# Kernel optimization log

Measured on AMD Instinct MI355X. Metric: run time of the kernel, lower is better.

The kernel has to match this reference:

```python
import jax, jax.numpy as jnp
import numpy as np

B, N_OBJS, HW = 2, 30, 64
W_H = HW * HW                      # 4096 visual tokens
N = W_H + 4 * N_OBJS + 64          # 4280 total tokens (satisfies the N - 4*n_objs - 64 == 64*64 check)
QUERY_DIM, HEADS, DIM_HEAD = 320, 8, 40
INNER = HEADS * DIM_HEAD


def setup_inputs() -> dict:
    key = jax.random.key(0)
    ks = jax.random.split(key, 7)
    x = jax.random.normal(ks[0], (B, N, QUERY_DIM), dtype=jnp.float32)
    # binary per-object instance masks on the 64x64 visual grid
    att_masks = (jax.random.uniform(ks[1], (B, N_OBJS, HW, HW)) < 0.15).astype(jnp.float32)
    s = 0.02
    Wq = jax.random.normal(ks[2], (QUERY_DIM, INNER), dtype=jnp.float32) * s
    Wk = jax.random.normal(ks[3], (QUERY_DIM, INNER), dtype=jnp.float32) * s
    Wv = jax.random.normal(ks[4], (QUERY_DIM, INNER), dtype=jnp.float32) * s
    Wo = jax.random.normal(ks[5], (INNER, QUERY_DIM), dtype=jnp.float32) * s
    bo = jax.random.normal(ks[6], (QUERY_DIM,), dtype=jnp.float32) * s
    return {"x": x, "att_masks": att_masks, "Wq": Wq, "Wk": Wk, "Wv": Wv, "Wo": Wo, "bo": bo}


def _build_mask(att_masks):
    # att_masks: [B, n_objs, 64, 64] -> additive/boolean grounding mask [B, 1, N, N]
    b, n_objs = att_masks.shape[0], att_masks.shape[1]
    m = att_masks.reshape(b, n_objs, W_H)                     # [B, O, 4096]
    # sum over objects of per-object outer products (bmm then sum over objs)
    ind = jnp.einsum('boi,boj->bij', m, m)                    # [B, 4096, 4096]
    # visual_token_masks ends up exactly 1 where ind>=1 else 0 (the two masked assigns)
    visual = (ind >= 1.0).astype(att_masks.dtype)
    mask = jnp.ones((b, 1, N, N), dtype=att_masks.dtype)
    mask = mask.at[:, :, :W_H, :W_H].set(visual[:, None])
    mr = m[:, None]                                           # [B, 1, O, 4096]
    rep_rows = jnp.tile(mr, (1, 1, 4, 1))                     # [B, 1, 4O, 4096]
    mask = mask.at[:, :, W_H:N - 64, :W_H].set(rep_rows)
    mask = mask.at[:, :, W_H + n_objs:W_H + 3 * n_objs, :W_H].set(1.0)
    rep_cols = jnp.tile(jnp.swapaxes(mr, 2, 3), (1, 1, 1, 4))  # [B, 1, 4096, 4O]
    mask = mask.at[:, :, :W_H, W_H:N - 64].set(rep_cols)
    mask = mask.at[:, :, :W_H, W_H + n_objs:W_H + 3 * n_objs].set(1.0)
    mask = mask + jnp.eye(N, dtype=att_masks.dtype)[None, None] * 1e-9
    return mask


def reference(x, att_masks, Wq, Wk, Wv, Wo, bo):
    b, n, _ = x.shape
    scale = DIM_HEAD ** -0.5
    q = (x @ Wq).reshape(b, n, HEADS, DIM_HEAD).transpose(0, 2, 1, 3)  # [B,H,N,C]
    k = (x @ Wk).reshape(b, n, HEADS, DIM_HEAD).transpose(0, 2, 1, 3)
    v = (x @ Wv).reshape(b, n, HEADS, DIM_HEAD).transpose(0, 2, 1, 3)
    mask = _build_mask(att_masks)                                      # [B,1,N,N]
    sim = jnp.einsum('bhic,bhjc->bhij', q, k) * scale                  # [B,H,N,N]
    sim = jnp.where(mask <= 0.0, -jnp.inf, sim)
    attn = jax.nn.softmax(sim, axis=-1)
    out = jnp.einsum('bhij,bhjc->bhic', attn, v)                       # [B,H,N,C]
    out = out.transpose(0, 2, 1, 3).reshape(b, n, INNER)
    return out @ Wo + bo
```

## Files before the change

kernel.cpp:

```cpp
#include <hip/hip_runtime.h>
#include <hip/hip_bf16.h>

#define BB 2
#define N_TOK 4280
#define NPAD 4352
#define MPAD 8576
#define WH 4096
#define NOBJ 30
#define QDIM 320
#define HEADS 8
#define DHEAD 40
#define M_ROWS (BB * N_TOK)
#define NT64 (NPAD / 64)
#define NQT (NPAD / 128)
#define KSPLIT 4
#define NTH (NT64 / KSPLIT)

typedef __attribute__((ext_vector_type(8))) short short8;
typedef __attribute__((ext_vector_type(4))) short short4v;
typedef __attribute__((ext_vector_type(4))) float f32x4;
typedef __attribute__((ext_vector_type(4))) unsigned uintx4;
typedef __attribute__((ext_vector_type(2))) unsigned long long u64x2;

#define GLD16(lds, g) __builtin_amdgcn_global_load_lds( \
    (const __attribute__((address_space(1))) unsigned*)(g), \
    (__attribute__((address_space(3))) unsigned*)(lds), 16, 0, 0)
#define GLD4(lds, g) __builtin_amdgcn_global_load_lds( \
    (const __attribute__((address_space(1))) unsigned*)(g), \
    (__attribute__((address_space(3))) unsigned*)(lds), 4, 0, 0)

__device__ __forceinline__ ushort f2bf(float x) {
    union { __hip_bfloat16 h; ushort u; } cv;
    cv.h = __float2bfloat16(x);
    return cv.u;
}
__device__ __forceinline__ float bf2f(ushort u) {
    union { unsigned u; float f; } cv;
    cv.u = ((unsigned)u) << 16;
    return cv.f;
}

__global__ void k_zero(u64x2* __restrict__ p, int n16) {
    int stride = gridDim.x * blockDim.x;
    u64x2 z = {0ull, 0ull};
    for (int i = blockIdx.x * blockDim.x + threadIdx.x; i < n16; i += stride)
        p[i] = z;
}

__global__ void k_bits(const float* __restrict__ att, unsigned* __restrict__ bits) {
    int gid = blockIdx.x * blockDim.x + threadIdx.x;
    if (gid >= BB * NPAD) return;
    int b = gid / NPAD, i = gid - b * NPAD;
    unsigned v = 0;
    if (i < WH) {
        const float* base = att + (size_t)b * NOBJ * WH + i;
        #pragma unroll
        for (int o = 0; o < NOBJ; ++o)
            if (base[(size_t)o * WH] > 0.5f) v |= (1u << o);
    }
    bits[gid] = v;
}

__global__ void k_xcvt(const float* __restrict__ x, ushort* __restrict__ xb) {
    int i = blockIdx.x * blockDim.x + threadIdx.x;
    if (i >= M_ROWS * QDIM / 8) return;
    float4 v0 = ((const float4*)x)[i * 2];
    float4 v1 = ((const float4*)x)[i * 2 + 1];
    short8 o;
    o[0] = (short)f2bf(v0.x); o[1] = (short)f2bf(v0.y);
    o[2] = (short)f2bf(v0.z); o[3] = (short)f2bf(v0.w);
    o[4] = (short)f2bf(v1.x); o[5] = (short)f2bf(v1.y);
    o[6] = (short)f2bf(v1.z); o[7] = (short)f2bf(v1.w);
    ((short8*)xb)[i] = o;
}

__global__ __launch_bounds__(256) void k_wcvt(const float* __restrict__ Wq,
                                              const float* __restrict__ Wk,
                                              const float* __restrict__ Wv,
                                              const float* __restrict__ Wo,
                                              ushort* __restrict__ WtAll) {
    __shared__ float T[32][33];
    const int k0 = blockIdx.x * 32;
    const int np0 = blockIdx.y * 32;
    const float SC = 0.15811388300841897f * 1.4426950408889634f;
    const float* src; int n0; float sc = 1.f;
    if (np0 < 320)      { src = Wq; n0 = np0;       sc = SC; }
    else if (np0 < 640) { src = Wk; n0 = np0 - 320; }
    else if (np0 < 960) { src = Wv; n0 = np0 - 640; }
    else                { src = Wo; n0 = np0 - 960; }
    const int tid = threadIdx.x;
    #pragma unroll
    for (int it = 0; it < 4; ++it) {
        int idx = tid + it * 256;
        int r = idx >> 5, c = idx & 31;
        T[r][c] = src[(size_t)(k0 + r) * QDIM + n0 + c];
    }
    __syncthreads();
    #pragma unroll
    for (int it = 0; it < 4; ++it) {
        int idx = tid + it * 256;
        int rr = idx >> 5, cc = idx & 31;
        WtAll[(size_t)(np0 + rr) * QDIM + k0 + cc] = f2bf(T[cc][rr] * sc);
    }
}

template<int IS_OUT>
__global__ __launch_bounds__(256) void k_mm(const ushort* __restrict__ A,
                                            const ushort* __restrict__ Wt,
                                            const float* __restrict__ bias,
                                            ushort* __restrict__ Qb,
                                            ushort* __restrict__ Kb,
                                            ushort* __restrict__ Vt,
                                            float* __restrict__ Cout) {
    __shared__ __align__(16) char Ab[2][8192];
    __shared__ __align__(16) char Bb[2][8192];
    const int tid = threadIdx.x, lane = tid & 63, wv = tid >> 6;
    const int g = lane >> 4, c16 = lane & 15, l7 = lane & 7;
    const int rsub = lane >> 3, slotx = lane & 7;
    const int m0 = blockIdx.x * 64;
    const int nt = blockIdx.y;

    f32x4 acc[4] = {{0,0,0,0},{0,0,0,0},{0,0,0,0},{0,0,0,0}};

    auto STAGE = [&](int ks, int bufi) {
        const int k0 = ks * 64;
        #pragma unroll
        for (int u = 0; u < 2; ++u) {
            int r0 = wv * 16 + u * 8;
            int row = r0 + rsub;
            int slot = slotx ^ (row & 7);
            GLD16(Ab[bufi] + r0 * 128, A + (size_t)(m0 + row) * QDIM + k0 + slot * 8);
            GLD16(Bb[bufi] + r0 * 128, Wt + (size_t)(nt * 64 + row) * QDIM + k0 + slot * 8);
        }
    };

    const int sl0 = (g ^ l7) * 16, sl1 = ((4 + g) ^ l7) * 16;

    STAGE(0, 0);
    __syncthreads();
    int cur = 0;
    for (int ks = 0; ks < 5; ++ks) {
        if (ks < 4) STAGE(ks + 1, cur ^ 1);
        const char* bbase = Bb[cur] + (wv * 16 + c16) * 128;
        short8 bf0 = *(const short8*)(bbase + sl0);
        short8 bf1 = *(const short8*)(bbase + sl1);
        #pragma unroll
        for (int mi = 0; mi < 4; ++mi) {
            const char* abase = Ab[cur] + (mi * 16 + c16) * 128;
            acc[mi] = __builtin_amdgcn_mfma_f32_16x16x32_bf16(*(const short8*)(abase + sl0), bf0, acc[mi], 0, 0, 0);
            acc[mi] = __builtin_amdgcn_mfma_f32_16x16x32_bf16(*(const short8*)(abase + sl1), bf1, acc[mi], 0, 0, 0);
        }
        __syncthreads();
        cur ^= 1;
    }

    const int ng = nt * 64 + wv * 16 + c16;
    if (IS_OUT) {
        float bv = bias[ng];
        #pragma unroll
        for (int mi = 0; mi < 4; ++mi)
            #pragma unroll
            for (int r = 0; r < 4; ++r) {
                int m = m0 + mi * 16 + g * 4 + r;
                if (m < M_ROWS) Cout[(size_t)m * QDIM + ng] = acc[mi][r] + bv;
            }
    } else {
        int p = ng / QDIM, nn = ng - p * QDIM;
        int h = nn / DHEAD, d = nn - h * DHEAD;
        if (p == 2) {
            #pragma unroll
            for (int mi = 0; mi < 4; ++mi) {
                int m = m0 + mi * 16 + g * 4;
                if (m >= M_ROWS) continue;
                int b = m / N_TOK, tok = m - b * N_TOK;
                short4v w4;
                w4[0] = (short)f2bf(acc[mi][0]);
                w4[1] = (short)f2bf(acc[mi][1]);
                w4[2] = (short)f2bf(acc[mi][2]);
                w4[3] = (short)f2bf(acc[mi][3]);
                *(short4v*)(Vt + ((size_t)(b * HEADS + h) * 48 + d) * NPAD + tok) = w4;
            }
        } else {
            ushort* base = (p == 0) ? Qb : Kb;
            #pragma unroll
            for (int mi = 0; mi < 4; ++mi)
                #pragma unroll
                for (int r = 0; r < 4; ++r) {
                    int m = m0 + mi * 16 + g * 4 + r;
                    if (m >= M_ROWS) continue;
                    int b = m / N_TOK, tok = m - b * N_TOK;
                    base[((size_t)(b * HEADS + h) * NPAD + tok) * 64 + d] = f2bf(acc[mi][r]);
                }
        }
    }
}

__global__ __launch_bounds__(256) void k_norm(const ushort* __restrict__ Qb,
                                              const ushort* __restrict__ Kb,
                                              float* __restrict__ Bsh) {
    __shared__ float rq[256], rk[256];
    const int bh = blockIdx.x, tid = threadIdx.x;
    float mq = 0.f, mk = 0.f;
    for (int tok = tid; tok < N_TOK; tok += 256) {
        const ushort* qp = Qb + ((size_t)bh * NPAD + tok) * 64;
        const ushort* kp = Kb + ((size_t)bh * NPAD + tok) * 64;
        float sq = 0.f, sk = 0.f;
        #pragma unroll
        for (int d8 = 0; d8 < 40; d8 += 8) {
            short8 a = *(const short8*)(qp + d8);
            short8 c = *(const short8*)(kp + d8);
            #pragma unroll
            for (int j = 0; j < 8; ++j) {
                float fa = bf2f((ushort)a[j]), fc = bf2f((ushort)c[j]);
                sq += fa * fa; sk += fc * fc;
            }
        }
        mq = fmaxf(mq, sq); mk = fmaxf(mk, sk);
    }
    rq[tid] = mq; rk[tid] = mk;
    __syncthreads();
    for (int s = 128; s > 0; s >>= 1) {
        if (tid < s) {
            rq[tid] = fmaxf(rq[tid], rq[tid + s]);
            rk[tid] = fmaxf(rk[tid], rk[tid + s]);
        }
        __syncthreads();
    }
    if (tid == 0) Bsh[bh] = sqrtf(rq[0]) * sqrtf(rk[0]);
}

__global__ void k_patch(ushort* __restrict__ Qb, ushort* __restrict__ Kb,
                        ushort* __restrict__ Vt, const float* __restrict__ Bsh) {
    int gid = blockIdx.x * blockDim.x + threadIdx.x;
    if (gid >= 16 * NPAD) return;
    int bh = gid / NPAD, tok = gid - bh * NPAD;
    float B = Bsh[bh];
    Qb[(size_t)gid * 64 + 40] = f2bf(-B);
    if (tok < N_TOK) Kb[(size_t)gid * 64 + 40] = (ushort)0x3F80;
    Vt[((size_t)bh * 48 + 40) * NPAD + tok] = (tok < N_TOK) ? (ushort)0x3F80 : (ushort)0;
}

__device__ __forceinline__ bool mask_ok(int i, int j, unsigned bi, unsigned bj) {
    if (j >= N_TOK) return false;
    if (i == j) return true;
    if (i < WH) {
        if (j < WH) return (bi & bj) != 0u;
        if (j >= WH + 4 * NOBJ) return true;
        int cI = j - WH;
        if ((unsigned)(cI - NOBJ) < (unsigned)(2 * NOBJ)) return true;
        int om = (cI < NOBJ) ? cI : cI - 3 * NOBJ;
        return ((bi >> om) & 1u) != 0u;
    }
    if (j >= WH) return true;
    if (i >= WH + 4 * NOBJ) return true;
    int rI = i - WH;
    if ((unsigned)(rI - NOBJ) < (unsigned)(2 * NOBJ)) return true;
    int om = (rI < NOBJ) ? rI : rI - 3 * NOBJ;
    return ((bj >> om) & 1u) != 0u;
}

__global__ __launch_bounds__(256, 4) void k_attn(const ushort* __restrict__ Qb,
                                                 const ushort* __restrict__ Kb,
                                                 const ushort* __restrict__ Vt,
                                                 const unsigned* __restrict__ bits,
                                                 float* __restrict__ Opart,
                                                 float* __restrict__ Lpart) {
    __shared__ __align__(16) char KtB[64 * 128];
    __shared__ __align__(16) char VtB[48 * 128];
    __shared__ __align__(16) char PsB[4 * 4096];
    __shared__ __align__(16) unsigned bJB[64];

    const int tid = threadIdx.x;
    const int lane = tid & 63, wv = tid >> 6;
    const int g = lane >> 4, c16 = lane & 15;
    const int l7x = c16 & 7;
    const int rsub = lane >> 3, slotx = lane & 7;

    const int bid = blockIdx.x;
    const int logical = (bid & 7) * 272 + (bid >> 3);
    const int grp = logical / NQT;
    const int qt = logical - grp * NQT;
    const int bh = grp >> 2, ks = grp & 3;
    const int b = bh >> 3;
    const int qb_blk = qt * 128;
    const int q0w = qb_blk + wv * 32;
    const int iqA = q0w + c16, iqB = iqA + 16;
    const bool vis_i = (qt < 32);
    const int t0 = ks * NTH;

    short8 qA0, qA1, qB0, qB1;
    {
        const ushort* qp = Qb + ((size_t)bh * NPAD + iqA) * 64 + g * 8;
        qA0 = *(const short8*)(qp);
        qA1 = *(const short8*)(qp + 32);
        qB0 = *(const short8*)(qp + 16 * 64);
        qB1 = *(const short8*)(qp + 16 * 64 + 32);
    }
    const unsigned bI_A = bits[(size_t)b * NPAD + iqA];
    const unsigned bI_B = bits[(size_t)b * NPAD + iqB];

    const ushort* kp = Kb + ((size_t)bh * NPAD + t0 * 64 + wv * 16 + rsub) * 64 + (slotx ^ rsub) * 8;
    const ushort* vbase = Vt + (size_t)bh * 48 * NPAD;
    int voff0 = 0, voff1 = 0;
    if (wv < 3) {
        int d0 = wv * 16 + rsub, d1 = d0 + 8;
        voff0 = d0 * NPAD + (slotx ^ rsub) * 8;
        voff1 = d1 * NPAD + (slotx ^ rsub) * 8;
    }
    const unsigned* bp = bits + (size_t)b * NPAD + t0 * 64 + lane;

    auto STAGE_K = [&](const ushort* kpt) {
        GLD16(KtB + (wv * 16) * 128, kpt);
        GLD16(KtB + (wv * 16 + 8) * 128, kpt + 512);
    };
    auto STAGE_V = [&](int j0) {
        if (wv < 3) {
            GLD16(VtB + (wv * 16) * 128, vbase + j0 + voff0);
            GLD16(VtB + (wv * 16 + 8) * 128, vbase + j0 + voff1);
        }
    };
    auto STAGE_B = [&](const unsigned* bpt) {
        if (wv == 3) GLD4(bJB, bpt);
    };

    const int sl0 = (g ^ l7x) * 16;
    const int sl1 = ((4 + g) ^ l7x) * 16;
    const int pswA = wv * 4096 + c16 * 128;
    const int pswB = pswA + 2048;
    const int swz = l7x << 4;

    f32x4 oA0 = {0,0,0,0}, oA1 = oA0, oA2 = oA0;
    f32x4 oB0 = oA0, oB1 = oA0, oB2 = oA0;

    STAGE_K(kp); STAGE_V(t0 * 64); STAGE_B(bp);
    __syncthreads();

    for (int t = 0; t < NTH; ++t) {
        const int tg = t0 + t;
        const int j0 = tg * 64;

        auto do_tile = [&](auto okA_fn, auto okB_fn) {
            #pragma unroll
            for (int kt = 0; kt < 4; ++kt) {
                const char* arow = KtB + (kt * 16 + c16) * 128;
                short8 a0 = *(const short8*)(arow + sl0);
                short8 a1 = *(const short8*)(arow + sl1);
                f32x4 sA = {0,0,0,0}, sB = {0,0,0,0};
                __builtin_amdgcn_s_setprio(1);
                sA = __builtin_amdgcn_mfma_f32_16x16x32_bf16(a0, qA0, sA, 0, 0, 0);
                sA = __builtin_amdgcn_mfma_f32_16x16x32_bf16(a1, qA1, sA, 0, 0, 0);
                sB = __builtin_amdgcn_mfma_f32_16x16x32_bf16(a0, qB0, sB, 0, 0, 0);
                sB = __builtin_amdgcn_mfma_f32_16x16x32_bf16(a1, qB1, sB, 0, 0, 0);
                __builtin_amdgcn_s_setprio(0);
                uintx4 bk = *(const uintx4*)&bJB[kt * 16 + g * 4];
                float pA[4], pB[4];
                #pragma unroll
                for (int r = 0; r < 4; ++r) {
                    int j = j0 + kt * 16 + g * 4 + r;
                    float eA = __builtin_amdgcn_exp2f(sA[r]);
                    float eB = __builtin_amdgcn_exp2f(sB[r]);
                    pA[r] = okA_fn(j, bk[r]) ? eA : 0.f;
                    pB[r] = okB_fn(j, bk[r]) ? eB : 0.f;
                }
                unsigned wA0, wA1, wB0, wB1;
                asm("v_cvt_pk_bf16_f32 %0, %1, %2" : "=v"(wA0) : "v"(pA[0]), "v"(pA[1]));
                asm("v_cvt_pk_bf16_f32 %0, %1, %2" : "=v"(wA1) : "v"(pA[2]), "v"(pA[3]));
                asm("v_cvt_pk_bf16_f32 %0, %1, %2" : "=v"(wB0) : "v"(pB[0]), "v"(pB[1]));
                asm("v_cvt_pk_bf16_f32 %0, %1, %2" : "=v"(wB1) : "v"(pB[2]), "v"(pB[3]));
                uint2 vA; vA.x = wA0; vA.y = wA1;
                uint2 vB; vB.x = wB0; vB.y = wB1;
                int po = (kt * 32 + g * 8) ^ swz;
                *(uint2*)(PsB + pswA + po) = vA;
                *(uint2*)(PsB + pswB + po) = vB;
            }
        };

        const bool vis_j = (j0 + 64 <= WH);
        if (vis_i && vis_j && ((tg >> 1) != qt)) {
            do_tile([&](int j, unsigned bj) { return (bI_A & bj) != 0u; },
                    [&](int j, unsigned bj) { return (bI_B & bj) != 0u; });
        } else if (vis_i && vis_j) {
            do_tile([&](int j, unsigned bj) { return ((bI_A & bj) != 0u) || (iqA == j); },
                    [&](int j, unsigned bj) { return ((bI_B & bj) != 0u) || (iqB == j); });
        } else {
            do_tile([&](int j, unsigned bj) { return mask_ok(iqA, j, bI_A, bj); },
                    [&](int j, unsigned bj) { return mask_ok(iqB, j, bI_B, bj); });
        }

        __syncthreads();
        kp += 64 * 64; bp += 64;
        if (t + 1 < NTH) { STAGE_K(kp); STAGE_B(bp); }

        short8 paA0 = *(const short8*)(PsB + pswA + sl0);
        short8 paA1 = *(const short8*)(PsB + pswA + sl1);
        short8 paB0 = *(const short8*)(PsB + pswB + sl0);
        short8 paB1 = *(const short8*)(PsB + pswB + sl1);
        {
            const char* v0r = VtB + (0 * 16 + c16) * 128;
            const char* v1r = VtB + (1 * 16 + c16) * 128;
            const char* v2r = VtB + (2 * 16 + c16) * 128;
            short8 v00 = *(const short8*)(v0r + sl0), v01 = *(const short8*)(v0r + sl1);
            short8 v10 = *(const short8*)(v1r + sl0), v11 = *(const short8*)(v1r + sl1);
            short8 v20 = *(const short8*)(v2r + sl0), v21 = *(const short8*)(v2r + sl1);
            __builtin_amdgcn_s_setprio(1);
            oA0 = __builtin_amdgcn_mfma_f32_16x16x32_bf16(paA0, v00, oA0, 0, 0, 0);
            oA0 = __builtin_amdgcn_mfma_f32_16x16x32_bf16(paA1, v01, oA0, 0, 0, 0);
            oB0 = __builtin_amdgcn_mfma_f32_16x16x32_bf16(paB0, v00, oB0, 0, 0, 0);
            oB0 = __builtin_amdgcn_mfma_f32_16x16x32_bf16(paB1, v01, oB0, 0, 0, 0);
            oA1 = __builtin_amdgcn_mfma_f32_16x16x32_bf16(paA0, v10, oA1, 0, 0, 0);
            oA1 = __builtin_amdgcn_mfma_f32_16x16x32_bf16(paA1, v11, oA1, 0, 0, 0);
            oB1 = __builtin_amdgcn_mfma_f32_16x16x32_bf16(paB0, v10, oB1, 0, 0, 0);
            oB1 = __builtin_amdgcn_mfma_f32_16x16x32_bf16(paB1, v11, oB1, 0, 0, 0);
            oA2 = __builtin_amdgcn_mfma_f32_16x16x32_bf16(paA0, v20, oA2, 0, 0, 0);
            oA2 = __builtin_amdgcn_mfma_f32_16x16x32_bf16(paA1, v21, oA2, 0, 0, 0);
            oB2 = __builtin_amdgcn_mfma_f32_16x16x32_bf16(paB0, v20, oB2, 0, 0, 0);
            oB2 = __builtin_amdgcn_mfma_f32_16x16x32_bf16(paB1, v21, oB2, 0, 0, 0);
            __builtin_amdgcn_s_setprio(0);
        }

        __syncthreads();
        if (t + 1 < NTH) STAGE_V((tg + 1) * 64);
    }

    const size_t prow = ((size_t)ks * 16 + bh) * NPAD;
    if (c16 == 8) {
        #pragma unroll
        for (int r = 0; r < 4; ++r) {
            Lpart[prow + q0w + g * 4 + r]      = oA2[r];
            Lpart[prow + q0w + 16 + g * 4 + r] = oB2[r];
        }
    }
    #pragma unroll
    for (int r = 0; r < 4; ++r) {
        int qrA = q0w + g * 4 + r;
        int qrB = qrA + 16;
        if (qrA < N_TOK) {
            float* dst = Opart + (prow + qrA) * 40;
            dst[c16]      = oA0[r];
            dst[16 + c16] = oA1[r];
            if (c16 < 8) dst[32 + c16] = oA2[r];
        }
        if (qrB < N_TOK) {
            float* dst = Opart + (prow + qrB) * 40;
            dst[c16]      = oB0[r];
            dst[16 + c16] = oB1[r];
            if (c16 < 8) dst[32 + c16] = oB2[r];
        }
    }
}

__global__ __launch_bounds__(256) void k_comb(const float* __restrict__ Opart,
                                              const float* __restrict__ Lpart,
                                              ushort* __restrict__ AOb) {
    int gid = blockIdx.x * blockDim.x + threadIdx.x;
    if (gid >= 16 * N_TOK * 10) return;
    int row = gid / 10, v = gid - row * 10;
    int bh = row / N_TOK, q = row - bh * N_TOK;
    f32x4 s = {0.f, 0.f, 0.f, 0.f};
    float l = 0.f;
    #pragma unroll
    for (int ks = 0; ks < KSPLIT; ++ks) {
        size_t rr = ((size_t)ks * 16 + bh) * NPAD + q;
        f32x4 a = *(const f32x4*)(Opart + rr * 40 + v * 4);
        s[0] += a[0]; s[1] += a[1]; s[2] += a[2]; s[3] += a[3];
        l += Lpart[rr];
    }
    float inv = 1.f / l;
    int b = bh >> 3, h = bh & 7;
    short4v o;
    o[0] = (short)f2bf(s[0] * inv);
    o[1] = (short)f2bf(s[1] * inv);
    o[2] = (short)f2bf(s[2] * inv);
    o[3] = (short)f2bf(s[3] * inv);
    *(short4v*)(AOb + (size_t)(b * N_TOK + q) * QDIM + h * DHEAD + v * 4) = o;
}

extern "C" void kernel_launch(void* const* d_in, const int* in_sizes, int n_in,
                              void* d_out, int out_size, void* d_ws, size_t ws_size,
                              hipStream_t stream) {
    const float* x   = (const float*)d_in[0];
    const float* att = (const float*)d_in[1];
    const float* Wq  = (const float*)d_in[2];
    const float* Wk  = (const float*)d_in[3];
    const float* Wv  = (const float*)d_in[4];
    const float* Wo  = (const float*)d_in[5];
    const float* bo  = (const float*)d_in[6];
    float* out = (float*)d_out;

    char* w = (char*)d_ws;
    unsigned* bits = (unsigned*)w;
    float* Bsh = (float*)(w + 40960);
    size_t off = 65536;
    ushort* xb    = (ushort*)(w + off); off += (size_t)MPAD * QDIM * 2;
    ushort* WtAll = (ushort*)(w + off); off += (size_t)1280 * QDIM * 2;
    ushort* Qb    = (ushort*)(w + off); off += (size_t)16 * NPAD * 64 * 2;
    ushort* Kb    = (ushort*)(w + off); off += (size_t)16 * NPAD * 64 * 2;
    ushort* Vt    = (ushort*)(w + off); off += (size_t)16 * 48 * NPAD * 2;
    ushort* AOb   = (ushort*)(w + off); off += (size_t)MPAD * QDIM * 2;
    float*  Opart = (float*)(w + off);  off += (size_t)KSPLIT * 16 * NPAD * 40 * 4;
    float*  Lpart = (float*)(w + off);

    k_zero<<<2048, 256, 0, stream>>>((u64x2*)Qb, (int)((size_t)2 * 16 * NPAD * 64 * 2 / 16));
    k_bits<<<(BB * NPAD + 255) / 256, 256, 0, stream>>>(att, bits);
    k_xcvt<<<(M_ROWS * QDIM / 8 + 255) / 256, 256, 0, stream>>>(x, xb);
    k_wcvt<<<dim3(10, 40), 256, 0, stream>>>(Wq, Wk, Wv, Wo, WtAll);

    k_mm<0><<<dim3(MPAD / 64, 15), 256, 0, stream>>>(xb, WtAll, nullptr, Qb, Kb, Vt, nullptr);
    k_norm<<<16, 256, 0, stream>>>(Qb, Kb, Bsh);
    k_patch<<<(16 * NPAD + 255) / 256, 256, 0, stream>>>(Qb, Kb, Vt, Bsh);
    k_attn<<<16 * NQT * KSPLIT, 256, 0, stream>>>(Qb, Kb, Vt, bits, Opart, Lpart);
    k_comb<<<(16 * N_TOK * 10 + 255) / 256, 256, 0, stream>>>(Opart, Lpart, AOb);
    k_mm<1><<<dim3(MPAD / 64, 5), 256, 0, stream>>>(AOb, WtAll + 960 * QDIM, bo,
                                                    nullptr, nullptr, nullptr, out);
}
```

Measured before the change: 209.4 us.

## Load K/V fragments directly from global in attention; split norm reduction with atomics

The attention kernel drops its LDS staging of K, V and mask bits, along with the per-tile __syncthreads barriers. Each wave now reads its MFMA operand fragments straight from global memory, relying on the L1/L2 caches for reuse across the four waves. The norm kernel is split from 16 to 128 blocks, which combine partial maxima through atomicMax on float bit patterns; the buffer is zeroed in k_bits. The trade is fewer barriers and less LDS traffic against redundant global loads per wave and exposed load latency, since nothing is prefetched anymore.

```diff
diff --git a/kernel.cpp b/kernel.cpp
--- a/kernel.cpp
+++ b/kernel.cpp
@@ -25,9 +25,6 @@
 #define GLD16(lds, g) __builtin_amdgcn_global_load_lds( \
     (const __attribute__((address_space(1))) unsigned*)(g), \
     (__attribute__((address_space(3))) unsigned*)(lds), 16, 0, 0)
-#define GLD4(lds, g) __builtin_amdgcn_global_load_lds( \
-    (const __attribute__((address_space(1))) unsigned*)(g), \
-    (__attribute__((address_space(3))) unsigned*)(lds), 4, 0, 0)
 
 __device__ __forceinline__ ushort f2bf(float x) {
     union { __hip_bfloat16 h; ushort u; } cv;
@@ -47,8 +44,10 @@
         p[i] = z;
 }
 
-__global__ void k_bits(const float* __restrict__ att, unsigned* __restrict__ bits) {
+__global__ void k_bits(const float* __restrict__ att, unsigned* __restrict__ bits,
+                       unsigned* __restrict__ MQK) {
     int gid = blockIdx.x * blockDim.x + threadIdx.x;
+    if (gid < 32) MQK[gid] = 0;
     if (gid >= BB * NPAD) return;
     int b = gid / NPAD, i = gid - b * NPAD;
     unsigned v = 0;
@@ -197,11 +196,12 @@
 
 __global__ __launch_bounds__(256) void k_norm(const ushort* __restrict__ Qb,
                                               const ushort* __restrict__ Kb,
-                                              float* __restrict__ Bsh) {
+                                              unsigned* __restrict__ MQK) {
     __shared__ float rq[256], rk[256];
-    const int bh = blockIdx.x, tid = threadIdx.x;
+    const int bh = blockIdx.x >> 3, part = blockIdx.x & 7;
+    const int tid = threadIdx.x;
     float mq = 0.f, mk = 0.f;
-    for (int tok = tid; tok < N_TOK; tok += 256) {
+    for (int tok = part * 256 + tid; tok < N_TOK; tok += 2048) {
         const ushort* qp = Qb + ((size_t)bh * NPAD + tok) * 64;
         const ushort* kp = Kb + ((size_t)bh * NPAD + tok) * 64;
         float sq = 0.f, sk = 0.f;
@@ -226,15 +226,18 @@
         }
         __syncthreads();
     }
-    if (tid == 0) Bsh[bh] = sqrtf(rq[0]) * sqrtf(rk[0]);
+    if (tid == 0) {
+        atomicMax(&MQK[bh],      __float_as_uint(rq[0]));
+        atomicMax(&MQK[16 + bh], __float_as_uint(rk[0]));
+    }
 }
 
 __global__ void k_patch(ushort* __restrict__ Qb, ushort* __restrict__ Kb,
-                        ushort* __restrict__ Vt, const float* __restrict__ Bsh) {
+                        ushort* __restrict__ Vt, const unsigned* __restrict__ MQK) {
     int gid = blockIdx.x * blockDim.x + threadIdx.x;
     if (gid >= 16 * NPAD) return;
     int bh = gid / NPAD, tok = gid - bh * NPAD;
-    float B = Bsh[bh];
+    float B = sqrtf(__uint_as_float(MQK[bh])) * sqrtf(__uint_as_float(MQK[16 + bh]));
     Qb[(size_t)gid * 64 + 40] = f2bf(-B);
     if (tok < N_TOK) Kb[(size_t)gid * 64 + 40] = (ushort)0x3F80;
     Vt[((size_t)bh * 48 + 40) * NPAD + tok] = (tok < N_TOK) ? (ushort)0x3F80 : (ushort)0;
@@ -265,16 +268,12 @@
                                                  const unsigned* __restrict__ bits,
                                                  float* __restrict__ Opart,
                                                  float* __restrict__ Lpart) {
-    __shared__ __align__(16) char KtB[64 * 128];
-    __shared__ __align__(16) char VtB[48 * 128];
     __shared__ __align__(16) char PsB[4 * 4096];
-    __shared__ __align__(16) unsigned bJB[64];
 
     const int tid = threadIdx.x;
     const int lane = tid & 63, wv = tid >> 6;
     const int g = lane >> 4, c16 = lane & 15;
     const int l7x = c16 & 7;
-    const int rsub = lane >> 3, slotx = lane & 7;
 
     const int bid = blockIdx.x;
     const int logical = (bid & 7) * 272 + (bid >> 3);
@@ -282,8 +281,7 @@
     const int qt = logical - grp * NQT;
     const int bh = grp >> 2, ks = grp & 3;
     const int b = bh >> 3;
-    const int qb_blk = qt * 128;
-    const int q0w = qb_blk + wv * 32;
+    const int q0w = qt * 128 + wv * 32;
     const int iqA = q0w + c16, iqB = iqA + 16;
     const bool vis_i = (qt < 32);
     const int t0 = ks * NTH;
@@ -299,41 +297,20 @@
     const unsigned bI_A = bits[(size_t)b * NPAD + iqA];
     const unsigned bI_B = bits[(size_t)b * NPAD + iqB];
 
-    const ushort* kp = Kb + ((size_t)bh * NPAD + t0 * 64 + wv * 16 + rsub) * 64 + (slotx ^ rsub) * 8;
-    const ushort* vbase = Vt + (size_t)bh * 48 * NPAD;
-    int voff0 = 0, voff1 = 0;
-    if (wv < 3) {
-        int d0 = wv * 16 + rsub, d1 = d0 + 8;
-        voff0 = d0 * NPAD + (slotx ^ rsub) * 8;
-        voff1 = d1 * NPAD + (slotx ^ rsub) * 8;
-    }
-    const unsigned* bp = bits + (size_t)b * NPAD + t0 * 64 + lane;
-
-    auto STAGE_K = [&](const ushort* kpt) {
-        GLD16(KtB + (wv * 16) * 128, kpt);
-        GLD16(KtB + (wv * 16 + 8) * 128, kpt + 512);
-    };
-    auto STAGE_V = [&](int j0) {
-        if (wv < 3) {
-            GLD16(VtB + (wv * 16) * 128, vbase + j0 + voff0);
-            GLD16(VtB + (wv * 16 + 8) * 128, vbase + j0 + voff1);
-        }
-    };
-    auto STAGE_B = [&](const unsigned* bpt) {
-        if (wv == 3) GLD4(bJB, bpt);
-    };
-
-    const int sl0 = (g ^ l7x) * 16;
-    const int sl1 = ((4 + g) ^ l7x) * 16;
+    const ushort* kc  = Kb + ((size_t)bh * NPAD + t0 * 64 + c16) * 64 + g * 8;
+    const ushort* v0p = Vt + ((size_t)bh * 48 +      c16) * NPAD + t0 * 64 + g * 8;
+    const ushort* v1p = v0p + (size_t)16 * NPAD;
+    const ushort* v2p = v1p + (size_t)16 * NPAD;
+    const unsigned* bq = bits + (size_t)b * NPAD + t0 * 64 + g * 4;
+
     const int pswA = wv * 4096 + c16 * 128;
     const int pswB = pswA + 2048;
     const int swz = l7x << 4;
+    const int sl0 = (g ^ l7x) * 16;
+    const int sl1 = ((4 + g) ^ l7x) * 16;
 
     f32x4 oA0 = {0,0,0,0}, oA1 = oA0, oA2 = oA0;
     f32x4 oB0 = oA0, oB1 = oA0, oB2 = oA0;
-
-    STAGE_K(kp); STAGE_V(t0 * 64); STAGE_B(bp);
-    __syncthreads();
 
     for (int t = 0; t < NTH; ++t) {
         const int tg = t0 + t;
@@ -342,9 +319,9 @@
         auto do_tile = [&](auto okA_fn, auto okB_fn) {
             #pragma unroll
             for (int kt = 0; kt < 4; ++kt) {
-                const char* arow = KtB + (kt * 16 + c16) * 128;
-                short8 a0 = *(const short8*)(arow + sl0);
-                short8 a1 = *(const short8*)(arow + sl1);
+                const ushort* krow = kc + kt * (16 * 64);
+                short8 a0 = *(const short8*)(krow);
+                short8 a1 = *(const short8*)(krow + 32);
                 f32x4 sA = {0,0,0,0}, sB = {0,0,0,0};
                 __builtin_amdgcn_s_setprio(1);
                 sA = __builtin_amdgcn_mfma_f32_16x16x32_bf16(a0, qA0, sA, 0, 0, 0);
@@ -352,7 +329,7 @@
                 sB = __builtin_amdgcn_mfma_f32_16x16x32_bf16(a0, qB0, sB, 0, 0, 0);
                 sB = __builtin_amdgcn_mfma_f32_16x16x32_bf16(a1, qB1, sB, 0, 0, 0);
                 __builtin_amdgcn_s_setprio(0);
-                uintx4 bk = *(const uintx4*)&bJB[kt * 16 + g * 4];
+                uintx4 bk = *(const uintx4*)(bq + kt * 16);
                 float pA[4], pB[4];
                 #pragma unroll
                 for (int r = 0; r < 4; ++r) {
@@ -387,21 +364,14 @@
                     [&](int j, unsigned bj) { return mask_ok(iqB, j, bI_B, bj); });
         }
 
-        __syncthreads();
-        kp += 64 * 64; bp += 64;
-        if (t + 1 < NTH) { STAGE_K(kp); STAGE_B(bp); }
-
         short8 paA0 = *(const short8*)(PsB + pswA + sl0);
         short8 paA1 = *(const short8*)(PsB + pswA + sl1);
         short8 paB0 = *(const short8*)(PsB + pswB + sl0);
         short8 paB1 = *(const short8*)(PsB + pswB + sl1);
         {
-            const char* v0r = VtB + (0 * 16 + c16) * 128;
-            const char* v1r = VtB + (1 * 16 + c16) * 128;
-            const char* v2r = VtB + (2 * 16 + c16) * 128;
-            short8 v00 = *(const short8*)(v0r + sl0), v01 = *(const short8*)(v0r + sl1);
-            short8 v10 = *(const short8*)(v1r + sl0), v11 = *(const short8*)(v1r + sl1);
-            short8 v20 = *(const short8*)(v2r + sl0), v21 = *(const short8*)(v2r + sl1);
+            short8 v00 = *(const short8*)(v0p), v01 = *(const short8*)(v0p + 32);
+            short8 v10 = *(const short8*)(v1p), v11 = *(const short8*)(v1p + 32);
+            short8 v20 = *(const short8*)(v2p), v21 = *(const short8*)(v2p + 32);
             __builtin_amdgcn_s_setprio(1);
             oA0 = __builtin_amdgcn_mfma_f32_16x16x32_bf16(paA0, v00, oA0, 0, 0, 0);
             oA0 = __builtin_amdgcn_mfma_f32_16x16x32_bf16(paA1, v01, oA0, 0, 0, 0);
@@ -418,8 +388,8 @@
             __builtin_amdgcn_s_setprio(0);
         }
 
-        __syncthreads();
-        if (t + 1 < NTH) STAGE_V((tg + 1) * 64);
+        kc += 64 * 64; bq += 64;
+        v0p += 64; v1p += 64; v2p += 64;
     }
 
     const size_t prow = ((size_t)ks * 16 + bh) * NPAD;
@@ -489,7 +459,7 @@
 
     char* w = (char*)d_ws;
     unsigned* bits = (unsigned*)w;
-    float* Bsh = (float*)(w + 40960);
+    unsigned* MQK = (unsigned*)(w + 40960);
     size_t off = 65536;
     ushort* xb    = (ushort*)(w + off); off += (size_t)MPAD * QDIM * 2;
     ushort* WtAll = (ushort*)(w + off); off += (size_t)1280 * QDIM * 2;
@@ -501,13 +471,13 @@
     float*  Lpart = (float*)(w + off);
 
     k_zero<<<2048, 256, 0, stream>>>((u64x2*)Qb, (int)((size_t)2 * 16 * NPAD * 64 * 2 / 16));
-    k_bits<<<(BB * NPAD + 255) / 256, 256, 0, stream>>>(att, bits);
+    k_bits<<<(BB * NPAD + 255) / 256, 256, 0, stream>>>(att, bits, MQK);
     k_xcvt<<<(M_ROWS * QDIM / 8 + 255) / 256, 256, 0, stream>>>(x, xb);
     k_wcvt<<<dim3(10, 40), 256, 0, stream>>>(Wq, Wk, Wv, Wo, WtAll);
 
     k_mm<0><<<dim3(MPAD / 64, 15), 256, 0, stream>>>(xb, WtAll, nullptr, Qb, Kb, Vt, nullptr);
-    k_norm<<<16, 256, 0, stream>>>(Qb, Kb, Bsh);
-    k_patch<<<(16 * NPAD + 255) / 256, 256, 0, stream>>>(Qb, Kb, Vt, Bsh);
+    k_norm<<<128, 256, 0, stream>>>(Qb, Kb, MQK);
+    k_patch<<<(16 * NPAD + 255) / 256, 256, 0, stream>>>(Qb, Kb, Vt, MQK);
     k_attn<<<16 * NQT * KSPLIT, 256, 0, stream>>>(Qb, Kb, Vt, bits, Opart, Lpart);
     k_comb<<<(16 * N_TOK * 10 + 255) / 256, 256, 0, stream>>>(Opart, Lpart, AOb);
     k_mm<1><<<dim3(MPAD / 64, 5), 256, 0, stream>>>(AOb, WtAll + 960 * QDIM, bo,
```

Result: slower. 372.5 us (+77.9%).

## Drop Q/K zero-fill, fuse prep kernels, parallelize norm reduction with atomics

Applied to the files above, without the earlier changes.

Removes the full memset of the Q and K buffers and instead zeroes only the K padding columns inside the patch kernel. It merges the mask-bit and x-conversion kernels into one launch that also clears the max accumulators. The norm reduction is split across 128 blocks, which combine their results through float-as-uint atomicMax instead of running as 16 serial blocks. The aim is to cut launch count, memset bandwidth and the serial reduction time. The risk is that Q padding columns 41-63 are no longer initialized, so leftover NaN garbage in the workspace could leak into the dot products.

```diff
diff --git a/kernel.cpp b/kernel.cpp
--- a/kernel.cpp
+++ b/kernel.cpp
@@ -20,7 +20,6 @@
 typedef __attribute__((ext_vector_type(4))) short short4v;
 typedef __attribute__((ext_vector_type(4))) float f32x4;
 typedef __attribute__((ext_vector_type(4))) unsigned uintx4;
-typedef __attribute__((ext_vector_type(2))) unsigned long long u64x2;
 
 #define GLD16(lds, g) __builtin_amdgcn_global_load_lds( \
     (const __attribute__((address_space(1))) unsigned*)(g), \
@@ -40,38 +39,31 @@
     return cv.f;
 }
 
-__global__ void k_zero(u64x2* __restrict__ p, int n16) {
-    int stride = gridDim.x * blockDim.x;
-    u64x2 z = {0ull, 0ull};
-    for (int i = blockIdx.x * blockDim.x + threadIdx.x; i < n16; i += stride)
-        p[i] = z;
-}
-
-__global__ void k_bits(const float* __restrict__ att, unsigned* __restrict__ bits) {
+__global__ void k_pre(const float* __restrict__ x, ushort* __restrict__ xb,
+                      const float* __restrict__ att, unsigned* __restrict__ bits,
+                      unsigned* __restrict__ MQK) {
     int gid = blockIdx.x * blockDim.x + threadIdx.x;
-    if (gid >= BB * NPAD) return;
-    int b = gid / NPAD, i = gid - b * NPAD;
-    unsigned v = 0;
-    if (i < WH) {
-        const float* base = att + (size_t)b * NOBJ * WH + i;
-        #pragma unroll
-        for (int o = 0; o < NOBJ; ++o)
-            if (base[(size_t)o * WH] > 0.5f) v |= (1u << o);
-    }
-    bits[gid] = v;
-}
-
-__global__ void k_xcvt(const float* __restrict__ x, ushort* __restrict__ xb) {
-    int i = blockIdx.x * blockDim.x + threadIdx.x;
-    if (i >= M_ROWS * QDIM / 8) return;
-    float4 v0 = ((const float4*)x)[i * 2];
-    float4 v1 = ((const float4*)x)[i * 2 + 1];
+    if (gid < 32) MQK[gid] = 0;
+    if (gid < BB * NPAD) {
+        int b = gid / NPAD, i = gid - b * NPAD;
+        unsigned v = 0;
+        if (i < WH) {
+            const float* base = att + (size_t)b * NOBJ * WH + i;
+            #pragma unroll
+            for (int o = 0; o < NOBJ; ++o)
+                if (base[(size_t)o * WH] > 0.5f) v |= (1u << o);
+        }
+        bits[gid] = v;
+    }
+    if (gid >= M_ROWS * QDIM / 8) return;
+    float4 v0 = ((const float4*)x)[gid * 2];
+    float4 v1 = ((const float4*)x)[gid * 2 + 1];
     short8 o;
     o[0] = (short)f2bf(v0.x); o[1] = (short)f2bf(v0.y);
     o[2] = (short)f2bf(v0.z); o[3] = (short)f2bf(v0.w);
     o[4] = (short)f2bf(v1.x); o[5] = (short)f2bf(v1.y);
     o[6] = (short)f2bf(v1.z); o[7] = (short)f2bf(v1.w);
-    ((short8*)xb)[i] = o;
+    ((short8*)xb)[gid] = o;
 }
 
 __global__ __launch_bounds__(256) void k_wcvt(const float* __restrict__ Wq,
@@ -197,11 +189,12 @@
 
 __global__ __launch_bounds__(256) void k_norm(const ushort* __restrict__ Qb,
                                               const ushort* __restrict__ Kb,
-                                              float* __restrict__ Bsh) {
+                                              unsigned* __restrict__ MQK) {
     __shared__ float rq[256], rk[256];
-    const int bh = blockIdx.x, tid = threadIdx.x;
+    const int bh = blockIdx.x >> 3, part = blockIdx.x & 7;
+    const int tid = threadIdx.x;
     float mq = 0.f, mk = 0.f;
-    for (int tok = tid; tok < N_TOK; tok += 256) {
+    for (int tok = part * 256 + tid; tok < N_TOK; tok += 2048) {
         const ushort* qp = Qb + ((size_t)bh * NPAD + tok) * 64;
         const ushort* kp = Kb + ((size_t)bh * NPAD + tok) * 64;
         float sq = 0.f, sk = 0.f;
@@ -226,17 +219,26 @@
         }
         __syncthreads();
     }
-    if (tid == 0) Bsh[bh] = sqrtf(rq[0]) * sqrtf(rk[0]);
+    if (tid == 0) {
+        atomicMax(&MQK[bh],      __float_as_uint(rq[0]));
+        atomicMax(&MQK[16 + bh], __float_as_uint(rk[0]));
+    }
 }
 
 __global__ void k_patch(ushort* __restrict__ Qb, ushort* __restrict__ Kb,
-                        ushort* __restrict__ Vt, const float* __restrict__ Bsh) {
+                        ushort* __restrict__ Vt, const unsigned* __restrict__ MQK) {
     int gid = blockIdx.x * blockDim.x + threadIdx.x;
     if (gid >= 16 * NPAD) return;
     int bh = gid / NPAD, tok = gid - bh * NPAD;
-    float B = Bsh[bh];
+    float B = sqrtf(__uint_as_float(MQK[bh])) * sqrtf(__uint_as_float(MQK[16 + bh]));
     Qb[(size_t)gid * 64 + 40] = f2bf(-B);
-    if (tok < N_TOK) Kb[(size_t)gid * 64 + 40] = (ushort)0x3F80;
+    short8 z = {0, 0, 0, 0, 0, 0, 0, 0};
+    short8 k1 = z;
+    k1[0] = (short)((tok < N_TOK) ? 0x3F80 : 0);
+    ushort* krow = Kb + (size_t)gid * 64;
+    *(short8*)(krow + 40) = k1;
+    *(short8*)(krow + 48) = z;
+    *(short8*)(krow + 56) = z;
     Vt[((size_t)bh * 48 + 40) * NPAD + tok] = (tok < N_TOK) ? (ushort)0x3F80 : (ushort)0;
 }
 
@@ -282,8 +284,7 @@
     const int qt = logical - grp * NQT;
     const int bh = grp >> 2, ks = grp & 3;
     const int b = bh >> 3;
-    const int qb_blk = qt * 128;
-    const int q0w = qb_blk + wv * 32;
+    const int q0w = qt * 128 + wv * 32;
     const int iqA = q0w + c16, iqB = iqA + 16;
     const bool vis_i = (qt < 32);
     const int t0 = ks * NTH;
@@ -489,7 +490,7 @@
 
     char* w = (char*)d_ws;
     unsigned* bits = (unsigned*)w;
-    float* Bsh = (float*)(w + 40960);
+    unsigned* MQK = (unsigned*)(w + 40960);
     size_t off = 65536;
     ushort* xb    = (ushort*)(w + off); off += (size_t)MPAD * QDIM * 2;
     ushort* WtAll = (ushort*)(w + off); off += (size_t)1280 * QDIM * 2;
@@ -500,14 +501,12 @@
     float*  Opart = (float*)(w + off);  off += (size_t)KSPLIT * 16 * NPAD * 40 * 4;
     float*  Lpart = (float*)(w + off);
 
-    k_zero<<<2048, 256, 0, stream>>>((u64x2*)Qb, (int)((size_t)2 * 16 * NPAD * 64 * 2 / 16));
-    k_bits<<<(BB * NPAD + 255) / 256, 256, 0, stream>>>(att, bits);
-    k_xcvt<<<(M_ROWS * QDIM / 8 + 255) / 256, 256, 0, stream>>>(x, xb);
+    k_pre<<<(M_ROWS * QDIM / 8 + 255) / 256, 256, 0, stream>>>(x, xb, att, bits, MQK);
     k_wcvt<<<dim3(10, 40), 256, 0, stream>>>(Wq, Wk, Wv, Wo, WtAll);
 
     k_mm<0><<<dim3(MPAD / 64, 15), 256, 0, stream>>>(xb, WtAll, nullptr, Qb, Kb, Vt, nullptr);
-    k_norm<<<16, 256, 0, stream>>>(Qb, Kb, Bsh);
-    k_patch<<<(16 * NPAD + 255) / 256, 256, 0, stream>>>(Qb, Kb, Vt, Bsh);
+    k_norm<<<128, 256, 0, stream>>>(Qb, Kb, MQK);
+    k_patch<<<(16 * NPAD + 255) / 256, 256, 0, stream>>>(Qb, Kb, Vt, MQK);
     k_attn<<<16 * NQT * KSPLIT, 256, 0, stream>>>(Qb, Kb, Vt, bits, Opart, Lpart);
     k_comb<<<(16 * N_TOK * 10 + 255) / 256, 256, 0, stream>>>(Opart, Lpart, AOb);
     k_mm<1><<<dim3(MPAD / 64, 5), 256, 0, stream>>>(AOb, WtAll + 960 * QDIM, bo,
```

Result: faster. 182.6 us (-12.8%).
